# Kernel optimization log

Hardware: AMD Instinct MI355X
Metric: run time of the kernel (lower is better)

Reference implementation:

```python
import jax, jax.numpy as jnp
import numpy as np

B, N, D = 8, 1024, 384
L, NH = 2, 8
HD = D // NH
HID2 = 4 * D  # project_in output channels = 2 * hidden = 2 * (2*dim) = 1536
HID = 2 * D  # GDFN hidden = 768


def setup_inputs() -> dict:
    key = jax.random.key(0)
    ks = jax.random.split(key, 16)
    s = 0.02
    return {
        "x": jax.random.normal(ks[0], (B, N, D), jnp.float32),
        "qkv_w": jax.random.normal(ks[1], (L, 3 * D, D), jnp.float32) * s,
        "qkv_b": jnp.zeros((L, 3 * D), jnp.float32),
        "proj_w": jax.random.normal(ks[2], (L, D, D), jnp.float32) * s,
        "proj_b": jnp.zeros((L, D), jnp.float32),
        "ln1_g": jnp.ones((L, D), jnp.float32),
        "ln1_b": jnp.zeros((L, D), jnp.float32),
        "ln2_g": jnp.ones((L, D), jnp.float32),
        "ln2_b": jnp.zeros((L, D), jnp.float32),
        "pin_w": jax.random.normal(ks[3], (L, HID2, D), jnp.float32) * s,
        "pin_b": jnp.zeros((L, HID2), jnp.float32),
        "dw_w": jax.random.normal(ks[4], (L, HID2, 1, 3, 3), jnp.float32) * s,
        "dw_b": jnp.zeros((L, HID2), jnp.float32),
        "pout_w": jax.random.normal(ks[5], (L, D, HID), jnp.float32) * s,
        "pout_b": jnp.zeros((L, D), jnp.float32),
    }


def _ln(y, g, b, eps=1e-5):
    m = y.mean(-1, keepdims=True)
    v = ((y - m) ** 2).mean(-1, keepdims=True)
    return (y - m) / jnp.sqrt(v + eps) * g + b


def _decay_bias(n, num_heads):
    # bias[h,i,j] = |i-j| * log(1 - 2^(-2 - 4*h/num_heads))  (negative)
    h = jnp.arange(num_heads, dtype=jnp.float32)
    decay = jnp.log(1.0 - 2.0 ** (-2.0 - 4.0 * h / num_heads))
    idx = jnp.arange(n, dtype=jnp.float32)
    dist = jnp.abs(idx[:, None] - idx[None, :])
    return dist[None] * decay[:, None, None]  # [NH, N, N]


def reference(x, qkv_w, qkv_b, proj_w, proj_b, ln1_g, ln1_b, ln2_g, ln2_b,
              pin_w, pin_b, dw_w, dw_b, pout_w, pout_b):
    b, n, d = x.shape
    hs = ws = int(np.sqrt(n))
    bias = _decay_bias(n, NH).astype(x.dtype)
    scale = HD ** -0.5
    nl = qkv_w.shape[0]
    for l in range(nl):
        # --- MHSA with spectral decay bias ---
        res = x
        xn = _ln(x, ln1_g[l], ln1_b[l])
        qkv = xn @ qkv_w[l].T + qkv_b[l]
        q, k, v = jnp.split(qkv, 3, axis=-1)
        q = q.reshape(b, n, NH, HD).transpose(0, 2, 1, 3)  # bhnd
        k = k.reshape(b, n, NH, HD).transpose(0, 2, 1, 3)
        v = v.reshape(b, n, NH, HD).transpose(0, 2, 1, 3)
        scores = jnp.einsum('bhnd,bhmd->bhnm', q, k) * scale + bias[None]
        attn = jax.nn.softmax(scores, axis=-1)
        out = jnp.einsum('bhnm,bhmd->bhnd', attn, v)
        out = out.transpose(0, 2, 1, 3).reshape(b, n, d)
        x = res + out @ proj_w[l].T + proj_b[l]
        # --- GDFN ---
        res = x
        xn = _ln(x, ln2_g[l], ln2_b[l])
        img = xn.transpose(0, 2, 1).reshape(b, d, hs, ws)  # NCHW
        h = jnp.einsum('oc,bchw->bohw', pin_w[l], img) + pin_b[l][None, :, None, None]
        h = jax.lax.conv_general_dilated(
            h, dw_w[l], window_strides=(1, 1), padding=[(1, 1), (1, 1)],
            feature_group_count=h.shape[1],
            dimension_numbers=('NCHW', 'OIHW', 'NCHW')) + dw_b[l][None, :, None, None]
        h1, h2 = jnp.split(h, 2, axis=1)
        g = jax.nn.gelu(h1, approximate=False) * h2
        o = jnp.einsum('oc,bchw->bohw', pout_w[l], g) + pout_b[l][None, :, None, None]
        x = res + o.reshape(b, d, n).transpose(0, 2, 1)
    return x
```

## Files before the change

kernel.cpp:

```cpp
#include <hip/hip_runtime.h>
#include <math.h>

#define B_ 8
#define N_ 1024
#define D_ 384
#define NH_ 8
#define HD_ 48
#define HID2_ 1536
#define HID_ 768
#define M_ (B_*N_)

typedef __attribute__((ext_vector_type(4))) float f32x4;
typedef __attribute__((ext_vector_type(2))) float f32x2;
typedef __attribute__((ext_vector_type(8))) short bf16x8;
typedef __attribute__((ext_vector_type(4))) short bf16x4;
typedef __attribute__((ext_vector_type(2))) unsigned u32x2;
typedef __attribute__((ext_vector_type(4))) unsigned u32x4;

__device__ inline unsigned short f2bf(float f) {
    unsigned u = __builtin_bit_cast(unsigned, f);
    u += 0x7fff + ((u >> 16) & 1);
    return (unsigned short)(u >> 16);
}
__device__ inline float bf2f(unsigned short h) {
    unsigned u = ((unsigned)h) << 16;
    return __builtin_bit_cast(float, u);
}
__device__ inline unsigned cvtpk_bf16(float lo, float hi) {
    unsigned r;
    asm("v_cvt_pk_bf16_f32 %0, %1, %2" : "=v"(r) : "v"(lo), "v"(hi));
    return r;
}
__device__ inline f32x4 mfma16(bf16x4 a, bf16x4 b, f32x4 c) {
#if __has_builtin(__builtin_amdgcn_mfma_f32_16x16x16bf16_1k)
    return __builtin_amdgcn_mfma_f32_16x16x16bf16_1k(a, b, c, 0, 0, 0);
#else
    asm("v_mfma_f32_16x16x16_bf16 %0, %1, %2, %0" : "+v"(c) : "v"(a), "v"(b));
    return c;
#endif
}

__global__ __launch_bounds__(256) void cvt4_kernel(
    const float* __restrict__ s1, const float* __restrict__ s2,
    const float* __restrict__ s3, const float* __restrict__ s4,
    int c1, int c2, int c3, int c4, unsigned short* __restrict__ out) {
    int i = blockIdx.x * 256 + threadIdx.x;
    if (i >= c1 + c2 + c3 + c4) return;
    const float* src; int off = i;
    float sc = 1.0f;
    if (i < c1) {
        src = s1;
        int row = (off * 4) / D_;
        if ((row % 1152) < 384) sc = 0.14433756729740643f * 1.4426950408889634f;
    }
    else if (i < c1 + c2) { src = s2; off = i - c1; }
    else if (i < c1 + c2 + c3) { src = s3; off = i - c1 - c2; }
    else { src = s4; off = i - c1 - c2 - c3; }
    f32x4 v = *(const f32x4*)(src + (size_t)off*4);
    ushort4 o;
    o.x = f2bf(v[0]*sc); o.y = f2bf(v[1]*sc);
    o.z = f2bf(v[2]*sc); o.w = f2bf(v[3]*sc);
    *(ushort4*)(out + (size_t)i*4) = o;
}

__global__ __launch_bounds__(256) void ln_kernel(
    const float* __restrict__ x, const float* __restrict__ g,
    const float* __restrict__ b, unsigned short* __restrict__ out) {
    int wave = threadIdx.x >> 6;
    int lane = threadIdx.x & 63;
    int row  = blockIdx.x * 4 + wave;
    const float* xr = x + (size_t)row * D_;
    f32x2 v[3];
    float s = 0.f;
    #pragma unroll
    for (int i = 0; i < 3; ++i) {
        v[i] = *(const f32x2*)(xr + i*128 + lane*2);
        s += v[i][0] + v[i][1];
    }
    #pragma unroll
    for (int off = 1; off < 64; off <<= 1) s += __shfl_xor(s, off);
    float mean = s * (1.0f/D_);
    float vs = 0.f;
    #pragma unroll
    for (int i = 0; i < 3; ++i) {
        float t0 = v[i][0]-mean, t1 = v[i][1]-mean;
        vs += t0*t0 + t1*t1;
    }
    #pragma unroll
    for (int off = 1; off < 64; off <<= 1) vs += __shfl_xor(vs, off);
    float rstd = rsqrtf(vs * (1.0f/D_) + 1e-5f);
    unsigned short* orow = out + (size_t)row * D_;
    #pragma unroll
    for (int i = 0; i < 3; ++i) {
        int d = i*128 + lane*2;
        ushort2 o;
        o.x = f2bf((v[i][0]-mean)*rstd*g[d]   + b[d]);
        o.y = f2bf((v[i][1]-mean)*rstd*g[d+1] + b[d+1]);
        *(ushort2*)(orow + d) = o;
    }
}

template<int MODE>
__global__ __launch_bounds__(256) void gemm_bf16(
    const unsigned short* __restrict__ A, const unsigned short* __restrict__ W,
    const float* __restrict__ bias, const float* __restrict__ res,
    void* __restrict__ outv, int M, int O, int K) {
    __shared__ unsigned short a_s[128][40];
    __shared__ unsigned short w_s[128][40];
    int tid = threadIdx.x;
    int o0 = blockIdx.x * 128;
    int m0 = blockIdx.y * 128;
    int wave = tid >> 6, lane = tid & 63;
    int wm = wave >> 1, wn = wave & 1;
    int lr = lane & 15, lc = lane >> 4;
    int r0 = tid >> 2, ch = tid & 3;
    int r1 = r0 + 64;
    f32x4 acc[4][4];
    #pragma unroll
    for (int i=0;i<4;++i)
      #pragma unroll
      for (int j=0;j<4;++j) acc[i][j] = (f32x4){0.f,0.f,0.f,0.f};

    const unsigned short* pa0 = A + (size_t)(m0+r0)*K + ch*8;
    const unsigned short* pa1 = A + (size_t)(m0+r1)*K + ch*8;
    const unsigned short* pw0 = W + (size_t)(o0+r0)*K + ch*8;
    const unsigned short* pw1 = W + (size_t)(o0+r1)*K + ch*8;
    bf16x8 a0 = *(const bf16x8*)pa0, a1 = *(const bf16x8*)pa1;
    bf16x8 w0 = *(const bf16x8*)pw0, w1 = *(const bf16x8*)pw1;

    for (int k0 = 0; k0 < K; k0 += 32) {
        __syncthreads();
        *(bf16x8*)&a_s[r0][ch*8] = a0;
        *(bf16x8*)&a_s[r1][ch*8] = a1;
        *(bf16x8*)&w_s[r0][ch*8] = w0;
        *(bf16x8*)&w_s[r1][ch*8] = w1;
        __syncthreads();
        if (k0 + 32 < K) {
            pa0 += 32; pa1 += 32; pw0 += 32; pw1 += 32;
            a0 = *(const bf16x8*)pa0; a1 = *(const bf16x8*)pa1;
            w0 = *(const bf16x8*)pw0; w1 = *(const bf16x8*)pw1;
        }
        bf16x8 af[4], wf[4];
        #pragma unroll
        for (int i = 0; i < 4; ++i)
            af[i] = *(const bf16x8*)&a_s[wm*64 + i*16 + lr][lc*8];
        #pragma unroll
        for (int j = 0; j < 4; ++j)
            wf[j] = *(const bf16x8*)&w_s[wn*64 + j*16 + lr][lc*8];
        #pragma unroll
        for (int i = 0; i < 4; ++i)
            #pragma unroll
            for (int j = 0; j < 4; ++j)
                acc[i][j] = __builtin_amdgcn_mfma_f32_16x16x32_bf16(
                    af[i], wf[j], acc[i][j], 0, 0, 0);
    }
    #pragma unroll
    for (int i = 0; i < 4; ++i) {
        int mbase = m0 + wm*64 + i*16 + lc*4;
        #pragma unroll
        for (int j = 0; j < 4; ++j) {
            int oc = o0 + wn*64 + j*16 + lr;
            float bv = bias[oc];
            #pragma unroll
            for (int r = 0; r < 4; ++r) {
                int m = mbase + r;
                float v = acc[i][j][r] + bv;
                if (MODE == 1) {
                    ((float*)outv)[(size_t)m*O + oc] = v + res[(size_t)m*O + oc];
                } else {
                    ((unsigned short*)outv)[(size_t)m*O + oc] = f2bf(v);
                }
            }
        }
    }
}

template<int MODE>
__global__ __launch_bounds__(256) void gemm_bf16_s(
    const unsigned short* __restrict__ A, const unsigned short* __restrict__ W,
    const float* __restrict__ bias, const float* __restrict__ res,
    void* __restrict__ outv, int M, int O, int K) {
    __shared__ unsigned short a_s[64][72];
    __shared__ unsigned short w_s[64][72];
    int tid = threadIdx.x;
    int o0 = blockIdx.x * 64;
    int m0 = blockIdx.y * 64;
    int wave = tid >> 6, lane = tid & 63;
    int lr = lane & 15, lc = lane >> 4;
    int r = tid >> 2, c = (tid & 3) * 16;
    f32x4 acc[4];
    #pragma unroll
    for (int i=0;i<4;++i) acc[i] = (f32x4){0.f,0.f,0.f,0.f};

    const unsigned short* pa = A + (size_t)(m0+r)*K + c;
    const unsigned short* pw = W + (size_t)(o0+r)*K + c;
    bf16x8 a0 = *(const bf16x8*)pa, a1 = *(const bf16x8*)(pa+8);
    bf16x8 w0 = *(const bf16x8*)pw, w1 = *(const bf16x8*)(pw+8);

    for (int k0 = 0; k0 < K; k0 += 64) {
        __syncthreads();
        *(bf16x8*)&a_s[r][c]   = a0;
        *(bf16x8*)&a_s[r][c+8] = a1;
        *(bf16x8*)&w_s[r][c]   = w0;
        *(bf16x8*)&w_s[r][c+8] = w1;
        __syncthreads();
        if (k0 + 64 < K) {
            pa += 64; pw += 64;
            a0 = *(const bf16x8*)pa; a1 = *(const bf16x8*)(pa+8);
            w0 = *(const bf16x8*)pw; w1 = *(const bf16x8*)(pw+8);
        }
        #pragma unroll
        for (int ks = 0; ks < 2; ++ks) {
            bf16x8 wf = *(const bf16x8*)&w_s[wave*16 + lr][ks*32 + lc*8];
            #pragma unroll
            for (int i = 0; i < 4; ++i) {
                bf16x8 af = *(const bf16x8*)&a_s[i*16 + lr][ks*32 + lc*8];
                acc[i] = __builtin_amdgcn_mfma_f32_16x16x32_bf16(af, wf, acc[i], 0,0,0);
            }
        }
    }
    int oc = o0 + wave*16 + lr;
    float bv = bias[oc];
    #pragma unroll
    for (int i = 0; i < 4; ++i) {
        #pragma unroll
        for (int rr = 0; rr < 4; ++rr) {
            int m = m0 + i*16 + lc*4 + rr;
            float v = acc[i][rr] + bv;
            if (MODE == 1) {
                ((float*)outv)[(size_t)m*O + oc] = v + res[(size_t)m*O + oc];
            } else {
                ((unsigned short*)outv)[(size_t)m*O + oc] = f2bf(v);
            }
        }
    }
}

__global__ __launch_bounds__(256) void attn_mfma(
    const unsigned short* __restrict__ qkv, unsigned short* __restrict__ out) {
    __shared__ unsigned short k_s[2][64][72];
    __shared__ unsigned short vt_s[2][48][72];
    int tid = threadIdx.x;
    int wave = tid >> 6, lane = tid & 63;
    int lr = lane & 15, lc = lane >> 4;
    int b = blockIdx.x >> 3, h = blockIdx.x & 7;
    int q0 = blockIdx.y * 64;
    const float LOG2E = 1.4426950408889634f;
    float decay_nats = logf(1.0f - exp2f(-2.0f - 0.5f*(float)h));
    float decay = decay_nats * LOG2E;
    const bf16x8 zero8 = {0,0,0,0,0,0,0,0};

    int bandi = (int)(20.0f / (-decay_nats));
    int lo = q0 - bandi - 63;
    int kt_lo = lo > 0 ? (lo >> 6) : 0;
    int kt_hi = (q0 + 63 + bandi) >> 6;
    if (kt_hi > 15) kt_hi = 15;

    if (tid < 192) {
        int zr = tid / 3, zc = 48 + (tid % 3) * 8;
        *(bf16x8*)&k_s[0][zr][zc] = zero8;
        *(bf16x8*)&k_s[1][zr][zc] = zero8;
    }

    int q = q0 + wave*16 + lr;
    float qqf = (float)q;
    const unsigned short* qrow = qkv + ((size_t)b*N_ + q)*1152 + h*48;
    bf16x8 qf0 = *(const bf16x8*)(qrow + lc*8);
    bf16x8 qf1 = zero8;
    if (lc < 2) qf1 = *(const bf16x8*)(qrow + 32 + lc*8);

    const unsigned short* kbase = qkv + (size_t)b*N_*1152 + D_ + h*48;
    int kr0 = tid / 6, kc0 = (tid % 6) * 8;
    bool kact1 = tid < 128;
    int s1 = kact1 ? tid + 256 : 0;
    int kr1 = s1 / 6, kc1 = (s1 % 6) * 8;
    const unsigned short* kp0 = kbase + (size_t)(kt_lo*64 + kr0)*1152 + kc0;
    const unsigned short* kp1 = kbase + (size_t)(kt_lo*64 + kr1)*1152 + kc1;

    int vd2 = (tid >> 3) * 2;
    int vch = tid & 7;
    bool vact = tid < 192;
    const unsigned short* vp = kbase + D_ + (size_t)(kt_lo*64 + vch*8)*1152 + vd2;

    bf16x8 rk0 = *(const bf16x8*)kp0;  kp0 += 64*1152;
    bf16x8 rk1 = zero8;
    if (kact1) rk1 = *(const bf16x8*)kp1;
    kp1 += 64*1152;
    unsigned rv[8];
    if (vact) {
        #pragma unroll
        for (int i = 0; i < 8; ++i)
            rv[i] = *(const unsigned*)(vp + (size_t)i*1152);
    }
    vp += 64*1152;

    float l_loc = 0.f;
    f32x4 oacc[3];
    #pragma unroll
    for (int i=0;i<3;++i) oacc[i] = (f32x4){0.f,0.f,0.f,0.f};

    int cur = 0;
    for (int kt = kt_lo; kt <= kt_hi; ++kt) {
        int n0 = kt * 64;
        *(bf16x8*)&k_s[cur][kr0][kc0] = rk0;
        if (kact1) *(bf16x8*)&k_s[cur][kr1][kc1] = rk1;
        if (vact) {
            u32x4 wlo, whi;
            #pragma unroll
            for (int i = 0; i < 4; ++i) {
                wlo[i] = (rv[2*i] & 0xffffu) | (rv[2*i+1] << 16);
                whi[i] = (rv[2*i] >> 16)    | (rv[2*i+1] & 0xffff0000u);
            }
            *(bf16x8*)&vt_s[cur][vd2]  [vch*8] = __builtin_bit_cast(bf16x8, wlo);
            *(bf16x8*)&vt_s[cur][vd2+1][vch*8] = __builtin_bit_cast(bf16x8, whi);
        }
        __syncthreads();
        if (kt < kt_hi) {
            rk0 = *(const bf16x8*)kp0;  kp0 += 64*1152;
            if (kact1) rk1 = *(const bf16x8*)kp1;
            kp1 += 64*1152;
            if (vact) {
                #pragma unroll
                for (int i = 0; i < 8; ++i)
                    rv[i] = *(const unsigned*)(vp + (size_t)i*1152);
            }
            vp += 64*1152;
        }
        f32x4 sc[4];
        #pragma unroll
        for (int f = 0; f < 4; ++f) {
            sc[f] = (f32x4){0.f,0.f,0.f,0.f};
            bf16x8 kf0 = *(const bf16x8*)&k_s[cur][f*16 + lr][lc*8];
            bf16x8 kf1 = *(const bf16x8*)&k_s[cur][f*16 + lr][32 + lc*8];
            sc[f] = __builtin_amdgcn_mfma_f32_16x16x32_bf16(kf0, qf0, sc[f],0,0,0);
            sc[f] = __builtin_amdgcn_mfma_f32_16x16x32_bf16(kf1, qf1, sc[f],0,0,0);
        }
        float base = qqf - (float)(n0 + lc*4);
        float p[4][4];
        #pragma unroll
        for (int f = 0; f < 4; ++f)
            #pragma unroll
            for (int r = 0; r < 4; ++r) {
                float d = base - (float)(f*16 + r);
                float s2 = fmaf(fabsf(d), decay, sc[f][r] - 16.0f);
                p[f][r] = __builtin_amdgcn_exp2f(s2);
                l_loc += p[f][r];
            }
        bf16x4 pfrag[4];
        #pragma unroll
        for (int f = 0; f < 4; ++f) {
            u32x2 u;
            u[0] = cvtpk_bf16(p[f][0], p[f][1]);
            u[1] = cvtpk_bf16(p[f][2], p[f][3]);
            pfrag[f] = __builtin_bit_cast(bf16x4, u);
        }
        #pragma unroll
        for (int f = 0; f < 4; ++f)
            #pragma unroll
            for (int md = 0; md < 3; ++md) {
                bf16x4 va = *(const bf16x4*)&vt_s[cur][md*16 + lr][f*16 + lc*4];
                oacc[md] = mfma16(va, pfrag[f], oacc[md]);
            }
        cur ^= 1;
    }
    float l = l_loc;
    l += __shfl_xor(l, 16);
    l += __shfl_xor(l, 32);
    float inv_l = 1.0f / l;
    #pragma unroll
    for (int md = 0; md < 3; ++md) {
        ushort4 o;
        o.x = f2bf(oacc[md][0]*inv_l);
        o.y = f2bf(oacc[md][1]*inv_l);
        o.z = f2bf(oacc[md][2]*inv_l);
        o.w = f2bf(oacc[md][3]*inv_l);
        *(ushort4*)(out + ((size_t)b*N_ + q)*D_ + h*48 + md*16 + lc*4) = o;
    }
}

__global__ __launch_bounds__(256) void dwconv_gate_bf16(
    const unsigned short* __restrict__ h, const float* __restrict__ dw_w,
    const float* __restrict__ dw_b, unsigned short* __restrict__ g) {
    __shared__ float wt_s[9][128];
    __shared__ float bs_s[128];
    int tid = threadIdx.x;
    int cg0 = blockIdx.x * 64;
    int y   = blockIdx.y;
    int b   = blockIdx.z;
    for (int i = tid; i < 1152; i += 256) {
        int tap = i >> 7, cl = i & 127;
        int gch = (cl < 64) ? (cg0 + cl) : (HID_ + cg0 + (cl - 64));
        wt_s[tap][cl] = dw_w[(size_t)gch*9 + tap];
    }
    if (tid < 128) {
        int gch = (tid < 64) ? (cg0 + tid) : (HID_ + cg0 + (tid - 64));
        bs_s[tid] = dw_b[gch];
    }
    __syncthreads();
    int x  = tid >> 3;
    int co = (tid & 7) * 8;
    int c1 = cg0 + co;
    const unsigned short* hb = h + (size_t)b*N_*HID2_;
    float acc1[8], acc2[8];
    #pragma unroll
    for (int j=0;j<8;++j) { acc1[j] = bs_s[co+j]; acc2[j] = bs_s[64+co+j]; }
    #pragma unroll
    for (int ky=0; ky<3; ++ky) {
        int yy = y + ky - 1;
        if (yy < 0 || yy >= 32) continue;
        #pragma unroll
        for (int kx=0; kx<3; ++kx) {
            int xx = x + kx - 1;
            if (xx < 0 || xx >= 32) continue;
            const unsigned short* p = hb + (size_t)(yy*32+xx)*HID2_ + c1;
            bf16x8 d1 = *(const bf16x8*)p;
            bf16x8 d2 = *(const bf16x8*)(p + HID_);
            int t = ky*3 + kx;
            f32x4 w1a = *(const f32x4*)&wt_s[t][co];
            f32x4 w1b = *(const f32x4*)&wt_s[t][co+4];
            f32x4 w2a = *(const f32x4*)&wt_s[t][64+co];
            f32x4 w2b = *(const f32x4*)&wt_s[t][64+co+4];
            #pragma unroll
            for (int j=0;j<4;++j) {
                acc1[j]   += bf2f((unsigned short)d1[j])   * w1a[j];
                acc1[j+4] += bf2f((unsigned short)d1[j+4]) * w1b[j];
                acc2[j]   += bf2f((unsigned short)d2[j])   * w2a[j];
                acc2[j+4] += bf2f((unsigned short)d2[j+4]) * w2b[j];
            }
        }
    }
    bf16x8 o;
    #pragma unroll
    for (int j=0;j<8;++j) {
        float ge = 0.5f*acc1[j]*(1.0f + erff(acc1[j]*0.70710678118f));
        o[j] = (short)f2bf(ge * acc2[j]);
    }
    *(bf16x8*)(g + (size_t)(b*N_ + y*32 + x)*HID_ + c1) = o;
}

extern "C" void kernel_launch(void* const* d_in, const int* in_sizes, int n_in,
                              void* d_out, int out_size, void* d_ws, size_t ws_size,
                              hipStream_t stream) {
    const float* x_in   = (const float*)d_in[0];
    const float* qkv_w  = (const float*)d_in[1];
    const float* qkv_b  = (const float*)d_in[2];
    const float* proj_w = (const float*)d_in[3];
    const float* proj_b = (const float*)d_in[4];
    const float* ln1_g  = (const float*)d_in[5];
    const float* ln1_b  = (const float*)d_in[6];
    const float* ln2_g  = (const float*)d_in[7];
    const float* ln2_b  = (const float*)d_in[8];
    const float* pin_w  = (const float*)d_in[9];
    const float* pin_b  = (const float*)d_in[10];
    const float* dw_w   = (const float*)d_in[11];
    const float* dw_b   = (const float*)d_in[12];
    const float* pout_w = (const float*)d_in[13];
    const float* pout_b = (const float*)d_in[14];

    float* pX = (float*)d_out;
    unsigned short* wXn  = (unsigned short*)d_ws;
    unsigned short* wQKV = wXn  + (size_t)M_*D_;
    unsigned short* wAO  = wQKV + (size_t)M_*3*D_;
    unsigned short* wH   = wAO  + (size_t)M_*D_;
    unsigned short* wG   = wH   + (size_t)M_*HID2_;
    unsigned short* wWq  = wG   + (size_t)M_*HID_;
    unsigned short* wWp  = wWq  + (size_t)2*3*D_*D_;
    unsigned short* wWi  = wWp  + (size_t)2*D_*D_;
    unsigned short* wWo  = wWi  + (size_t)2*HID2_*D_;

    int c1 = 2*3*D_*D_/4, c2 = 2*D_*D_/4, c3 = 2*HID2_*D_/4, c4 = 2*D_*HID_/4;
    int ctot = c1 + c2 + c3 + c4;
    cvt4_kernel<<<(ctot+255)/256, 256, 0, stream>>>(
        qkv_w, proj_w, pin_w, pout_w, c1, c2, c3, c4, wWq);

    hipMemcpyAsync(pX, x_in, sizeof(float)*(size_t)M_*D_,
                   hipMemcpyDeviceToDevice, stream);

    for (int l = 0; l < 2; ++l) {
        ln_kernel<<<M_/4, 256, 0, stream>>>(pX, ln1_g + l*D_, ln1_b + l*D_, wXn);
        gemm_bf16<0><<<dim3((3*D_)/128, M_/128), 256, 0, stream>>>(
            wXn, wWq + (size_t)l*3*D_*D_, qkv_b + (size_t)l*3*D_,
            nullptr, wQKV, M_, 3*D_, D_);
        attn_mfma<<<dim3(B_*NH_, N_/64), 256, 0, stream>>>(wQKV, wAO);
        gemm_bf16_s<1><<<dim3(D_/64, M_/64), 256, 0, stream>>>(
            wAO, wWp + (size_t)l*D_*D_, proj_b + (size_t)l*D_,
            pX, pX, M_, D_, D_);
        ln_kernel<<<M_/4, 256, 0, stream>>>(pX, ln2_g + l*D_, ln2_b + l*D_, wXn);
        gemm_bf16<0><<<dim3(HID2_/128, M_/128), 256, 0, stream>>>(
            wXn, wWi + (size_t)l*HID2_*D_, pin_b + (size_t)l*HID2_,
            nullptr, wH, M_, HID2_, D_);
        dwconv_gate_bf16<<<dim3(HID_/64, 32, B_), 256, 0, stream>>>(
            wH, dw_w + (size_t)l*HID2_*9, dw_b + (size_t)l*HID2_, wG);
        gemm_bf16_s<1><<<dim3(D_/64, M_/64), 256, 0, stream>>>(
            wG, wWo + (size_t)l*D_*HID_, pout_b + (size_t)l*D_,
            pX, pX, M_, D_, HID_);
    }
}
```

Baseline: 269.2 us.

## Double-buffer GEMM tiles via direct global-to-LDS loads; move q scaling into attention

The bf16 GEMM now loads A and W tiles straight into LDS with global_load_lds, ping-ponging between two buffers. This drops the register staging and one barrier per k-step, so the next tile's loads overlap the current MFMAs. The LDS rows lose their padding (stride 32 instead of 40), which may bring bank conflicts on the fragment reads, and correctness depends on the async LDS writes being waited on before the barrier. Separately, the softmax scale and log2e factor are no longer folded into the bf16 qkv weights; an extra fma in the attention score loop applies them instead.

```diff
diff --git a/kernel.cpp b/kernel.cpp
--- a/kernel.cpp
+++ b/kernel.cpp
@@ -39,6 +39,12 @@
     return c;
 #endif
 }
+__device__ inline void gld_lds16(const unsigned short* g, unsigned short* l) {
+    __builtin_amdgcn_global_load_lds(
+        (const __attribute__((address_space(1))) unsigned int*)(const void*)g,
+        (__attribute__((address_space(3))) unsigned int*)(void*)l,
+        16, 0, 0);
+}
 
 __global__ __launch_bounds__(256) void cvt4_kernel(
     const float* __restrict__ s1, const float* __restrict__ s2,
@@ -47,19 +53,13 @@
     int i = blockIdx.x * 256 + threadIdx.x;
     if (i >= c1 + c2 + c3 + c4) return;
     const float* src; int off = i;
-    float sc = 1.0f;
-    if (i < c1) {
-        src = s1;
-        int row = (off * 4) / D_;
-        if ((row % 1152) < 384) sc = 0.14433756729740643f * 1.4426950408889634f;
-    }
+    if (i < c1) { src = s1; }
     else if (i < c1 + c2) { src = s2; off = i - c1; }
     else if (i < c1 + c2 + c3) { src = s3; off = i - c1 - c2; }
     else { src = s4; off = i - c1 - c2 - c3; }
     f32x4 v = *(const f32x4*)(src + (size_t)off*4);
     ushort4 o;
-    o.x = f2bf(v[0]*sc); o.y = f2bf(v[1]*sc);
-    o.z = f2bf(v[2]*sc); o.w = f2bf(v[3]*sc);
+    o.x = f2bf(v[0]); o.y = f2bf(v[1]); o.z = f2bf(v[2]); o.w = f2bf(v[3]);
     *(ushort4*)(out + (size_t)i*4) = o;
 }
 
@@ -105,8 +105,8 @@
     const unsigned short* __restrict__ A, const unsigned short* __restrict__ W,
     const float* __restrict__ bias, const float* __restrict__ res,
     void* __restrict__ outv, int M, int O, int K) {
-    __shared__ unsigned short a_s[128][40];
-    __shared__ unsigned short w_s[128][40];
+    __shared__ unsigned short a_s[2][128*32];
+    __shared__ unsigned short w_s[2][128*32];
     int tid = threadIdx.x;
     int o0 = blockIdx.x * 128;
     int m0 = blockIdx.y * 128;
@@ -114,7 +114,7 @@
     int wm = wave >> 1, wn = wave & 1;
     int lr = lane & 15, lc = lane >> 4;
     int r0 = tid >> 2, ch = tid & 3;
-    int r1 = r0 + 64;
+    int ldso = r0*32 + ch*8;
     f32x4 acc[4][4];
     #pragma unroll
     for (int i=0;i<4;++i)
@@ -122,37 +122,41 @@
       for (int j=0;j<4;++j) acc[i][j] = (f32x4){0.f,0.f,0.f,0.f};
 
     const unsigned short* pa0 = A + (size_t)(m0+r0)*K + ch*8;
-    const unsigned short* pa1 = A + (size_t)(m0+r1)*K + ch*8;
+    const unsigned short* pa1 = A + (size_t)(m0+r0+64)*K + ch*8;
     const unsigned short* pw0 = W + (size_t)(o0+r0)*K + ch*8;
-    const unsigned short* pw1 = W + (size_t)(o0+r1)*K + ch*8;
-    bf16x8 a0 = *(const bf16x8*)pa0, a1 = *(const bf16x8*)pa1;
-    bf16x8 w0 = *(const bf16x8*)pw0, w1 = *(const bf16x8*)pw1;
-
+    const unsigned short* pw1 = W + (size_t)(o0+r0+64)*K + ch*8;
+
+    gld_lds16(pa0, &a_s[0][ldso]);
+    gld_lds16(pa1, &a_s[0][64*32 + ldso]);
+    gld_lds16(pw0, &w_s[0][ldso]);
+    gld_lds16(pw1, &w_s[0][64*32 + ldso]);
+    pa0 += 32; pa1 += 32; pw0 += 32; pw1 += 32;
+
+    int buf = 0;
     for (int k0 = 0; k0 < K; k0 += 32) {
         __syncthreads();
-        *(bf16x8*)&a_s[r0][ch*8] = a0;
-        *(bf16x8*)&a_s[r1][ch*8] = a1;
-        *(bf16x8*)&w_s[r0][ch*8] = w0;
-        *(bf16x8*)&w_s[r1][ch*8] = w1;
-        __syncthreads();
         if (k0 + 32 < K) {
+            int nb = buf ^ 1;
+            gld_lds16(pa0, &a_s[nb][ldso]);
+            gld_lds16(pa1, &a_s[nb][64*32 + ldso]);
+            gld_lds16(pw0, &w_s[nb][ldso]);
+            gld_lds16(pw1, &w_s[nb][64*32 + ldso]);
             pa0 += 32; pa1 += 32; pw0 += 32; pw1 += 32;
-            a0 = *(const bf16x8*)pa0; a1 = *(const bf16x8*)pa1;
-            w0 = *(const bf16x8*)pw0; w1 = *(const bf16x8*)pw1;
         }
         bf16x8 af[4], wf[4];
         #pragma unroll
         for (int i = 0; i < 4; ++i)
-            af[i] = *(const bf16x8*)&a_s[wm*64 + i*16 + lr][lc*8];
+            af[i] = *(const bf16x8*)&a_s[buf][(wm*64 + i*16 + lr)*32 + lc*8];
         #pragma unroll
         for (int j = 0; j < 4; ++j)
-            wf[j] = *(const bf16x8*)&w_s[wn*64 + j*16 + lr][lc*8];
+            wf[j] = *(const bf16x8*)&w_s[buf][(wn*64 + j*16 + lr)*32 + lc*8];
         #pragma unroll
         for (int i = 0; i < 4; ++i)
             #pragma unroll
             for (int j = 0; j < 4; ++j)
                 acc[i][j] = __builtin_amdgcn_mfma_f32_16x16x32_bf16(
                     af[i], wf[j], acc[i][j], 0, 0, 0);
+        buf ^= 1;
     }
     #pragma unroll
     for (int i = 0; i < 4; ++i) {
@@ -248,6 +252,7 @@
     const float LOG2E = 1.4426950408889634f;
     float decay_nats = logf(1.0f - exp2f(-2.0f - 0.5f*(float)h));
     float decay = decay_nats * LOG2E;
+    const float scale2 = 0.14433756729740643f * LOG2E;
     const bf16x8 zero8 = {0,0,0,0,0,0,0,0};
 
     int bandi = (int)(20.0f / (-decay_nats));
@@ -342,7 +347,8 @@
             #pragma unroll
             for (int r = 0; r < 4; ++r) {
                 float d = base - (float)(f*16 + r);
-                float s2 = fmaf(fabsf(d), decay, sc[f][r] - 16.0f);
+                float s2 = fmaf(fabsf(d), decay,
+                                fmaf(sc[f][r], scale2, -16.0f));
                 p[f][r] = __builtin_amdgcn_exp2f(s2);
                 l_loc += p[f][r];
             }
```

After: 271.9 us. No clear change (+1.0%).
